# Kernel tuning notes

Measured on AMD Instinct MI355X. Metric: run time of the kernel, lower is better.

## Reference

```python
import jax, jax.numpy as jnp
import numpy as np

N = 100000   # nodes
E = 800000   # edges
F_IN = 16
H = 64       # hidden_dim
L = 4        # num_layers
CD = 8       # contrastive_dim
BN_EPS = 1e-5


def setup_inputs() -> dict:
    key = jax.random.key(0)
    ks = jax.random.split(key, 20)
    s = 0.05
    return {
        "x": jax.random.normal(ks[0], (N, F_IN), jnp.float32),
        "edge_index": jax.random.randint(ks[1], (2, E), 0, N, jnp.int64),
        "batch": jnp.zeros((N,), jnp.int64),
        "enc_w1": jax.random.normal(ks[2], (F_IN, H), jnp.float32) * s,
        "enc_b1": jnp.zeros((H,), jnp.float32),
        "enc_w2": jax.random.normal(ks[3], (H, H), jnp.float32) * s,
        "enc_b2": jnp.zeros((H,), jnp.float32),
        "conv_w": jax.random.normal(ks[4], (L, 2 * H, H), jnp.float32) * s,
        "conv_b": jnp.zeros((L, H), jnp.float32),
        "bn_gamma": jnp.ones((L, H), jnp.float32),
        "bn_beta": jnp.zeros((L, H), jnp.float32),
        "out_w1": jax.random.normal(ks[5], (H, 64), jnp.float32) * s,
        "out_b1": jnp.zeros((64,), jnp.float32),
        "out_w2": jax.random.normal(ks[6], (64, 32), jnp.float32) * s,
        "out_b2": jnp.zeros((32,), jnp.float32),
        "out_w3": jax.random.normal(ks[7], (32, CD), jnp.float32) * s,
        "out_b3": jnp.zeros((CD,), jnp.float32),
    }


def _forward(x, edge_index, enc_w1, enc_b1, enc_w2, enc_b2,
             conv_w, conv_b, bn_gamma, bn_beta,
             out_w1, out_b1, out_w2, out_b2, out_w3, out_b3):
    row, col = edge_index[0], edge_index[1]
    # lc_encode: Linear+ELU, Linear+ELU
    h = jax.nn.elu(x @ enc_w1 + enc_b1)
    feats = jax.nn.elu(h @ enc_w2 + enc_b2)  # (N, H)

    ones = jnp.ones((E, 1), feats.dtype)
    counts = jnp.clip(jax.ops.segment_sum(ones, row, num_segments=N), 1.0)  # (N,1)
    bn_scale = 1.0 / jnp.sqrt(1.0 + BN_EPS)  # eval-mode BN: running_mean=0, running_var=1

    for i in range(L):
        xc = feats[row]               # gather centers (E, H)
        xn = feats[col]               # gather neighbors (E, H)
        ef = jnp.concatenate([xc, xn - xc], axis=-1)      # (E, 2H)
        e = jax.nn.elu(ef @ conv_w[i] + conv_b[i])        # Linear + ELU
        e = (e * bn_scale) * bn_gamma[i] + bn_beta[i]     # BatchNorm (eval); Dropout is identity
        agg = jax.ops.segment_sum(e, row, num_segments=N) / counts
        feats = agg + feats  # residual in Net.forward

    # output head (Dropout identity in eval)
    o = jax.nn.elu(feats @ out_w1 + out_b1)
    o = jax.nn.elu(o @ out_w2 + out_b2)
    return o @ out_w3 + out_b3  # (N, CD)


def reference(x, edge_index, batch, enc_w1, enc_b1, enc_w2, enc_b2,
              conv_w, conv_b, bn_gamma, bn_beta,
              out_w1, out_b1, out_w2, out_b2, out_w3, out_b3):
    out = _forward(x, edge_index, enc_w1, enc_b1, enc_w2, enc_b2,
                   conv_w, conv_b, bn_gamma, bn_beta,
                   out_w1, out_b1, out_w2, out_b2, out_w3, out_b3)
    return (out, batch)
```

## Files before the change

kernel.cpp:

```cpp
#include <hip/hip_runtime.h>

#define NN 100000
#define NE 800000
#define FIN 16
#define H 64
#define NL 4
#define CDIM 8
#define NT 1563
#define ROWS_PER_OWN 12500
#define ECHUNK 2048
#define NCHUNK ((NE + ECHUNK - 1) / ECHUNK)
#define CAP 32
#define HOT 8
#define SPILL (CAP - HOT)

__device__ __forceinline__ float elu(float x) { return x > 0.f ? x : __expf(x) - 1.f; }
__device__ __forceinline__ float4 elu4(float4 v) {
    return make_float4(elu(v.x), elu(v.y), elu(v.z), elu(v.w));
}

__device__ __forceinline__ unsigned short f2bf(float x) {
    union { float f; unsigned int u; } v; v.f = x;
    unsigned int r = v.u + 0x7fffu + ((v.u >> 16) & 1u);
    return (unsigned short)(r >> 16);
}
__device__ __forceinline__ float u2f(unsigned int u) {
    union { unsigned int u; float f; } v; v.u = u;
    return v.f;
}

__global__ __launch_bounds__(256) void k_scatter(const int* __restrict__ row,
                                                 const int* __restrict__ col,
                                                 int* cnt, int* __restrict__ hot,
                                                 int* __restrict__ spill) {
    int owner = blockIdx.x & 7;
    int chunk = blockIdx.x >> 3;
    int lo = owner * ROWS_PER_OWN, hi = lo + ROWS_PER_OWN;
    int base = chunk * ECHUNK;
    int end = base + ECHUNK; if (end > NE) end = NE;
    for (int e = base + threadIdx.x; e < end; e += 256) {
        int r = row[e];
        if (r >= lo && r < hi) {
            int p = atomicAdd(&cnt[r], 1);
            if (p < HOT) hot[(size_t)r * HOT + p] = col[e];
            else if (p < CAP) spill[(size_t)r * SPILL + (p - HOT)] = col[e];
        }
    }
}

__global__ __launch_bounds__(256) void k_enc(const float* __restrict__ x,
                                             const float* __restrict__ w1,
                                             const float* __restrict__ b1,
                                             const float* __restrict__ w2,
                                             const float* __restrict__ b2,
                                             float* __restrict__ feats,
                                             int* __restrict__ cnt) {
    __shared__ __align__(16) float xs[64 * 16];
    __shared__ __align__(16) float w1s[16 * 64];
    __shared__ __align__(16) float ws[64 * 64];
    __shared__ __align__(16) float fs[64 * 68];
    int tid = threadIdx.x;
    int base = blockIdx.x * 64;
    {
        int gid = blockIdx.x * 256 + tid;
        if (gid < NN) cnt[gid] = 0;
    }
    {
        size_t ei = (size_t)base * FIN + tid * 4;
        size_t emax = (size_t)NN * FIN - 4;
        if (ei > emax) ei = emax;
        *(float4*)&xs[tid * 4] = *(const float4*)&x[ei];
    }
    ((float4*)w1s)[tid] = ((const float4*)w1)[tid];
#pragma unroll
    for (int r = 0; r < 4; r++) ((float4*)ws)[tid + 256 * r] = ((const float4*)w2)[tid + 256 * r];
    __syncthreads();

    int wave = tid >> 6, j = tid & 63;
    float bb1 = b1[j];
    for (int i = 0; i < 16; i++) {
        int nl = i * 4 + wave;
        float acc = bb1;
#pragma unroll
        for (int k = 0; k < FIN; k++) acc += xs[nl * FIN + k] * w1s[k * 64 + j];
        fs[nl * 68 + j] = elu(acc);
    }
    __syncthreads();

    int cg = tid & 15, ng = tid >> 4;
    int c0 = cg * 4;
    float4 bb = ((const float4*)b2)[cg];
    float4 acc[4];
    acc[0] = bb; acc[1] = bb; acc[2] = bb; acc[3] = bb;
#pragma unroll 2
    for (int kq = 0; kq < 16; kq++) {
        int k0 = kq * 4;
        float4 w0 = *(const float4*)&ws[(k0 + 0) * 64 + c0];
        float4 w1v = *(const float4*)&ws[(k0 + 1) * 64 + c0];
        float4 w2v = *(const float4*)&ws[(k0 + 2) * 64 + c0];
        float4 w3v = *(const float4*)&ws[(k0 + 3) * 64 + c0];
#pragma unroll
        for (int m = 0; m < 4; m++) {
            float4 f = *(const float4*)&fs[(ng * 4 + m) * 68 + k0];
            acc[m].x += f.x * w0.x + f.y * w1v.x + f.z * w2v.x + f.w * w3v.x;
            acc[m].y += f.x * w0.y + f.y * w1v.y + f.z * w2v.y + f.w * w3v.y;
            acc[m].z += f.x * w0.z + f.y * w1v.z + f.z * w2v.z + f.w * w3v.z;
            acc[m].w += f.x * w0.w + f.y * w1v.w + f.z * w2v.w + f.w * w3v.w;
        }
    }
#pragma unroll
    for (int m = 0; m < 4; m++) {
        int n = base + ng * 4 + m;
        if (n < NN) *(float4*)&feats[(size_t)n * 64 + c0] = elu4(acc[m]);
    }
}

__global__ __launch_bounds__(256) void k_ab(const float* __restrict__ feats,
                                            const float* __restrict__ convw,
                                            const float* __restrict__ convb,
                                            unsigned short* __restrict__ Am,
                                            unsigned short* __restrict__ Bm) {
    __shared__ __align__(16) float fs[64 * 68];
    __shared__ __align__(16) float was[64 * 64];
    __shared__ __align__(16) float wbs[64 * 64];
    int tid = threadIdx.x;
    int base = blockIdx.x * 64;
#pragma unroll
    for (int r = 0; r < 4; r++) {
        int idx = tid + 256 * r;
        float4 wt = ((const float4*)convw)[idx];
        float4 wb = ((const float4*)convw)[1024 + idx];
        ((float4*)was)[idx] = make_float4(wt.x - wb.x, wt.y - wb.y, wt.z - wb.z, wt.w - wb.w);
        ((float4*)wbs)[idx] = wb;
        int rw = idx >> 4, cc = idx & 15;
        int n = base + rw; if (n >= NN) n = NN - 1;
        *(float4*)&fs[rw * 68 + cc * 4] = *(const float4*)&feats[(size_t)n * 64 + cc * 4];
    }
    __syncthreads();
    int cg = tid & 15, ng = tid >> 4;
    int c0 = cg * 4;
    float4 cb = ((const float4*)convb)[cg];
    float4 z = make_float4(0.f, 0.f, 0.f, 0.f);
    float4 accA[4], accB[4];
    accA[0] = cb; accA[1] = cb; accA[2] = cb; accA[3] = cb;
    accB[0] = z; accB[1] = z; accB[2] = z; accB[3] = z;
#pragma unroll 1
    for (int kq = 0; kq < 16; kq++) {
        int k0 = kq * 4;
        float4 a0 = *(const float4*)&was[(k0 + 0) * 64 + c0];
        float4 a1 = *(const float4*)&was[(k0 + 1) * 64 + c0];
        float4 a2 = *(const float4*)&was[(k0 + 2) * 64 + c0];
        float4 a3 = *(const float4*)&was[(k0 + 3) * 64 + c0];
        float4 b0 = *(const float4*)&wbs[(k0 + 0) * 64 + c0];
        float4 b1v = *(const float4*)&wbs[(k0 + 1) * 64 + c0];
        float4 b2v = *(const float4*)&wbs[(k0 + 2) * 64 + c0];
        float4 b3v = *(const float4*)&wbs[(k0 + 3) * 64 + c0];
#pragma unroll
        for (int m = 0; m < 4; m++) {
            float4 f = *(const float4*)&fs[(ng * 4 + m) * 68 + k0];
            accA[m].x += f.x * a0.x + f.y * a1.x + f.z * a2.x + f.w * a3.x;
            accA[m].y += f.x * a0.y + f.y * a1.y + f.z * a2.y + f.w * a3.y;
            accA[m].z += f.x * a0.z + f.y * a1.z + f.z * a2.z + f.w * a3.z;
            accA[m].w += f.x * a0.w + f.y * a1.w + f.z * a2.w + f.w * a3.w;
            accB[m].x += f.x * b0.x + f.y * b1v.x + f.z * b2v.x + f.w * b3v.x;
            accB[m].y += f.x * b0.y + f.y * b1v.y + f.z * b2v.y + f.w * b3v.y;
            accB[m].z += f.x * b0.z + f.y * b1v.z + f.z * b2v.z + f.w * b3v.z;
            accB[m].w += f.x * b0.w + f.y * b1v.w + f.z * b2v.w + f.w * b3v.w;
        }
    }
#pragma unroll
    for (int m = 0; m < 4; m++) {
        int n = base + ng * 4 + m;
        if (n < NN) {
            ushort4 pa, pb;
            pa.x = f2bf(accA[m].x); pa.y = f2bf(accA[m].y);
            pa.z = f2bf(accA[m].z); pa.w = f2bf(accA[m].w);
            pb.x = f2bf(accB[m].x); pb.y = f2bf(accB[m].y);
            pb.z = f2bf(accB[m].z); pb.w = f2bf(accB[m].w);
            *(ushort4*)&Am[(size_t)n * 64 + c0] = pa;
            *(ushort4*)&Bm[(size_t)n * 64 + c0] = pb;
        }
    }
}

__global__ __launch_bounds__(256) void k_gather(const unsigned short* __restrict__ Am,
                                                const unsigned short* __restrict__ Bm,
                                                const int* __restrict__ cnt,
                                                const int* __restrict__ hot,
                                                const int* __restrict__ spill,
                                                const float* __restrict__ gamma,
                                                const float* __restrict__ beta,
                                                float* __restrict__ feats) {
    int tid = threadIdx.x;
    int wave = tid >> 6, lane = tid & 63;
    int half = lane >> 5, l = lane & 31;
    int n = blockIdx.x * 8 + wave * 2 + half;
    int g = l >> 3;
    int cq = l & 7, c0 = cq * 8;
    int deg = cnt[n];
    if (deg > CAP) deg = CAP;
    int mycol = (l < HOT) ? hot[(size_t)n * HOT + l]
                          : spill[(size_t)n * SPILL + (l - HOT)];
    uint4 rawA = *(const uint4*)&Am[(size_t)n * H + c0];
    float4 a0 = make_float4(u2f(rawA.x << 16), u2f(rawA.x & 0xffff0000u),
                            u2f(rawA.y << 16), u2f(rawA.y & 0xffff0000u));
    float4 a1 = make_float4(u2f(rawA.z << 16), u2f(rawA.z & 0xffff0000u),
                            u2f(rawA.w << 16), u2f(rawA.w & 0xffff0000u));
    float4 f0, f1;
    if (g == 0) {
        f0 = *(const float4*)&feats[(size_t)n * H + c0];
        f1 = *(const float4*)&feats[(size_t)n * H + c0 + 4];
    }
    float4 acc0 = make_float4(0.f, 0.f, 0.f, 0.f);
    float4 acc1 = make_float4(0.f, 0.f, 0.f, 0.f);
    for (int p0 = 0; p0 < deg; p0 += 4) {
        int p = p0 + g;
        bool valid = p < deg;
        int pc = valid ? p : (deg - 1);
        int c = __shfl(mycol, (half << 5) + pc);
        uint4 raw = *(const uint4*)&Bm[(size_t)c * H + c0];
        float4 b0 = make_float4(u2f(raw.x << 16), u2f(raw.x & 0xffff0000u),
                                u2f(raw.y << 16), u2f(raw.y & 0xffff0000u));
        float4 b1 = make_float4(u2f(raw.z << 16), u2f(raw.z & 0xffff0000u),
                                u2f(raw.w << 16), u2f(raw.w & 0xffff0000u));
        float4 v0 = elu4(make_float4(a0.x + b0.x, a0.y + b0.y, a0.z + b0.z, a0.w + b0.w));
        float4 v1 = elu4(make_float4(a1.x + b1.x, a1.y + b1.y, a1.z + b1.z, a1.w + b1.w));
        if (valid) {
            acc0.x += v0.x; acc0.y += v0.y; acc0.z += v0.z; acc0.w += v0.w;
            acc1.x += v1.x; acc1.y += v1.y; acc1.z += v1.z; acc1.w += v1.w;
        }
    }
#pragma unroll
    for (int d = 8; d < 32; d <<= 1) {
        acc0.x += __shfl_xor(acc0.x, d); acc0.y += __shfl_xor(acc0.y, d);
        acc0.z += __shfl_xor(acc0.z, d); acc0.w += __shfl_xor(acc0.w, d);
        acc1.x += __shfl_xor(acc1.x, d); acc1.y += __shfl_xor(acc1.y, d);
        acc1.z += __shfl_xor(acc1.z, d); acc1.w += __shfl_xor(acc1.w, d);
    }
    if (g == 0 && deg > 0) {
        const float bs = 0.99999500003749968750f;
        float inv = bs / (float)deg;
        float4 gm0 = *(const float4*)&gamma[c0];
        float4 gm1 = *(const float4*)&gamma[c0 + 4];
        float4 bt0 = *(const float4*)&beta[c0];
        float4 bt1 = *(const float4*)&beta[c0 + 4];
        f0.x += acc0.x * gm0.x * inv + bt0.x;
        f0.y += acc0.y * gm0.y * inv + bt0.y;
        f0.z += acc0.z * gm0.z * inv + bt0.z;
        f0.w += acc0.w * gm0.w * inv + bt0.w;
        f1.x += acc1.x * gm1.x * inv + bt1.x;
        f1.y += acc1.y * gm1.y * inv + bt1.y;
        f1.z += acc1.z * gm1.z * inv + bt1.z;
        f1.w += acc1.w * gm1.w * inv + bt1.w;
        *(float4*)&feats[(size_t)n * H + c0] = f0;
        *(float4*)&feats[(size_t)n * H + c0 + 4] = f1;
    }
}

__global__ __launch_bounds__(256) void k_head(const float* __restrict__ feats,
                                              const float* __restrict__ w1,
                                              const float* __restrict__ b1,
                                              const float* __restrict__ w2,
                                              const float* __restrict__ b2,
                                              const float* __restrict__ w3,
                                              const float* __restrict__ b3,
                                              const int* __restrict__ batch,
                                              float* __restrict__ out,
                                              float* __restrict__ out2) {
    __shared__ __align__(16) float fs[64 * 68];
    __shared__ __align__(16) float w1s[64 * 64];
    __shared__ __align__(16) float o1s[64 * 68];
    __shared__ __align__(16) float w2s[64 * 32];
    __shared__ __align__(16) float w3s[32 * 8];
    int tid = threadIdx.x;
    int base = blockIdx.x * 64;
#pragma unroll
    for (int r = 0; r < 4; r++) {
        int idx = tid + 256 * r;
        ((float4*)w1s)[idx] = ((const float4*)w1)[idx];
        int rw = idx >> 4, cc = idx & 15;
        int n = base + rw; if (n >= NN) n = NN - 1;
        *(float4*)&fs[rw * 68 + cc * 4] = *(const float4*)&feats[(size_t)n * 64 + cc * 4];
    }
    ((float4*)w2s)[tid] = ((const float4*)w2)[tid];
    ((float4*)w2s)[tid + 256] = ((const float4*)w2)[tid + 256];
    if (tid < 64) ((float4*)w3s)[tid] = ((const float4*)w3)[tid];
    if (tid < 64) {
        int n = base + tid;
        if (n < NN) out2[n] = (float)batch[n];
    }
    __syncthreads();

    int cg = tid & 15, ng = tid >> 4;
    int c0 = cg * 4;
    {
        float4 bb = ((const float4*)b1)[cg];
        float4 acc[4];
        acc[0] = bb; acc[1] = bb; acc[2] = bb; acc[3] = bb;
#pragma unroll 2
        for (int kq = 0; kq < 16; kq++) {
            int k0 = kq * 4;
            float4 w0 = *(const float4*)&w1s[(k0 + 0) * 64 + c0];
            float4 w1v = *(const float4*)&w1s[(k0 + 1) * 64 + c0];
            float4 w2v = *(const float4*)&w1s[(k0 + 2) * 64 + c0];
            float4 w3v = *(const float4*)&w1s[(k0 + 3) * 64 + c0];
#pragma unroll
            for (int m = 0; m < 4; m++) {
                float4 f = *(const float4*)&fs[(ng * 4 + m) * 68 + k0];
                acc[m].x += f.x * w0.x + f.y * w1v.x + f.z * w2v.x + f.w * w3v.x;
                acc[m].y += f.x * w0.y + f.y * w1v.y + f.z * w2v.y + f.w * w3v.y;
                acc[m].z += f.x * w0.z + f.y * w1v.z + f.z * w2v.z + f.w * w3v.z;
                acc[m].w += f.x * w0.w + f.y * w1v.w + f.z * w2v.w + f.w * w3v.w;
            }
        }
        __syncthreads();
#pragma unroll
        for (int m = 0; m < 4; m++)
            *(float4*)&o1s[(ng * 4 + m) * 68 + c0] = elu4(acc[m]);
    }
    __syncthreads();

    float* o2s = fs;
    {
        int cg2 = tid & 7, ng2 = tid >> 3;
        int c20 = cg2 * 4;
        float4 bb = ((const float4*)b2)[cg2];
        float4 acc[2];
        acc[0] = bb; acc[1] = bb;
#pragma unroll 2
        for (int kq = 0; kq < 16; kq++) {
            int k0 = kq * 4;
            float4 w0 = *(const float4*)&w2s[(k0 + 0) * 32 + c20];
            float4 w1v = *(const float4*)&w2s[(k0 + 1) * 32 + c20];
            float4 w2v = *(const float4*)&w2s[(k0 + 2) * 32 + c20];
            float4 w3v = *(const float4*)&w2s[(k0 + 3) * 32 + c20];
#pragma unroll
            for (int m = 0; m < 2; m++) {
                float4 f = *(const float4*)&o1s[(ng2 * 2 + m) * 68 + k0];
                acc[m].x += f.x * w0.x + f.y * w1v.x + f.z * w2v.x + f.w * w3v.x;
                acc[m].y += f.x * w0.y + f.y * w1v.y + f.z * w2v.y + f.w * w3v.y;
                acc[m].z += f.x * w0.z + f.y * w1v.z + f.z * w2v.z + f.w * w3v.z;
                acc[m].w += f.x * w0.w + f.y * w1v.w + f.z * w2v.w + f.w * w3v.w;
            }
        }
#pragma unroll
        for (int m = 0; m < 2; m++)
            *(float4*)&o2s[(ng2 * 2 + m) * 40 + c20] = elu4(acc[m]);
    }
    __syncthreads();

    if (tid < 128) {
        int n3 = tid >> 1, c30 = (tid & 1) * 4;
        float4 acc = ((const float4*)b3)[tid & 1];
#pragma unroll 2
        for (int kq = 0; kq < 8; kq++) {
            int k0 = kq * 4;
            float4 w0 = *(const float4*)&w3s[(k0 + 0) * 8 + c30];
            float4 w1v = *(const float4*)&w3s[(k0 + 1) * 8 + c30];
            float4 w2v = *(const float4*)&w3s[(k0 + 2) * 8 + c30];
            float4 w3v = *(const float4*)&w3s[(k0 + 3) * 8 + c30];
            float4 f = *(const float4*)&o2s[n3 * 40 + k0];
            acc.x += f.x * w0.x + f.y * w1v.x + f.z * w2v.x + f.w * w3v.x;
            acc.y += f.x * w0.y + f.y * w1v.y + f.z * w2v.y + f.w * w3v.y;
            acc.z += f.x * w0.z + f.y * w1v.z + f.z * w2v.z + f.w * w3v.z;
            acc.w += f.x * w0.w + f.y * w1v.w + f.z * w2v.w + f.w * w3v.w;
        }
        int n = base + n3;
        if (n < NN) *(float4*)&out[(size_t)n * 8 + c30] = acc;
    }
}

extern "C" void kernel_launch(void* const* d_in, const int* in_sizes, int n_in,
                              void* d_out, int out_size, void* d_ws, size_t ws_size,
                              hipStream_t stream) {
    const float* x = (const float*)d_in[0];
    const int* edge_index = (const int*)d_in[1];
    const int* batch = (const int*)d_in[2];
    const float* enc_w1 = (const float*)d_in[3];
    const float* enc_b1 = (const float*)d_in[4];
    const float* enc_w2 = (const float*)d_in[5];
    const float* enc_b2 = (const float*)d_in[6];
    const float* conv_w = (const float*)d_in[7];
    const float* conv_b = (const float*)d_in[8];
    const float* bn_gamma = (const float*)d_in[9];
    const float* bn_beta = (const float*)d_in[10];
    const float* out_w1 = (const float*)d_in[11];
    const float* out_b1 = (const float*)d_in[12];
    const float* out_w2 = (const float*)d_in[13];
    const float* out_b2 = (const float*)d_in[14];
    const float* out_w3 = (const float*)d_in[15];
    const float* out_b3 = (const float*)d_in[16];

    const int* row = edge_index;
    const int* col = edge_index + NE;

    float* feats = (float*)d_ws;
    unsigned short* Abuf = (unsigned short*)(feats + (size_t)NN * H);
    unsigned short* Bbuf = Abuf + (size_t)NN * H;
    int* cnt = (int*)(Bbuf + (size_t)NN * H);
    int* hot = cnt + NN;
    int* spill = hot + (size_t)NN * HOT;

    float* out = (float*)d_out;

    k_enc<<<NT, 256, 0, stream>>>(x, enc_w1, enc_b1, enc_w2, enc_b2, feats, cnt);
    k_scatter<<<NCHUNK * 8, 256, 0, stream>>>(row, col, cnt, hot, spill);

    for (int i = 0; i < NL; i++) {
        k_ab<<<NT, 256, 0, stream>>>(feats, conv_w + (size_t)i * 2 * H * H,
                                     conv_b + (size_t)i * H, Abuf, Bbuf);
        k_gather<<<NN / 8, 256, 0, stream>>>(Abuf, Bbuf, cnt, hot, spill,
                                             bn_gamma + (size_t)i * H,
                                             bn_beta + (size_t)i * H, feats);
    }

    k_head<<<NT, 256, 0, stream>>>(feats, out_w1, out_b1, out_w2, out_b2,
                                   out_w3, out_b3, batch, out,
                                   out + (size_t)NN * CDIM);
}
```

Before: 416.2 us.

## Compute per-node A/B projections with bf16 MFMA using pre-transposed weights

Weight differencing and transposition into a bf16 layout are precomputed once for all layers by extra blocks appended to the scatter kernel. The per-layer node projection kernel then runs 16x16x32 bf16 MFMA instructions with weights held in registers, instead of fp32 FMAs over shared memory tiles. It processes 128 nodes per block, has no shared-memory staging or block barrier, and converts feats to bf16 on the fly. This is meant to cut the ALU and LDS cost of the dense projection. It adds bf16 rounding of inputs and weights before accumulation.

```diff
diff --git a/kernel.cpp b/kernel.cpp
--- a/kernel.cpp
+++ b/kernel.cpp
@@ -7,6 +7,7 @@
 #define NL 4
 #define CDIM 8
 #define NT 1563
+#define NAB 782
 #define ROWS_PER_OWN 12500
 #define ECHUNK 2048
 #define NCHUNK ((NE + ECHUNK - 1) / ECHUNK)
@@ -14,6 +15,9 @@
 #define HOT 8
 #define SPILL (CAP - HOT)
 
+typedef __attribute__((ext_vector_type(8))) short bf16x8;
+typedef __attribute__((ext_vector_type(4))) float f32x4;
+
 __device__ __forceinline__ float elu(float x) { return x > 0.f ? x : __expf(x) - 1.f; }
 __device__ __forceinline__ float4 elu4(float4 v) {
     return make_float4(elu(v.x), elu(v.y), elu(v.z), elu(v.w));
@@ -32,7 +36,28 @@
 __global__ __launch_bounds__(256) void k_scatter(const int* __restrict__ row,
                                                  const int* __restrict__ col,
                                                  int* cnt, int* __restrict__ hot,
-                                                 int* __restrict__ spill) {
+                                                 int* __restrict__ spill,
+                                                 const float* __restrict__ convw,
+                                                 unsigned short* __restrict__ WT) {
+    if (blockIdx.x >= NCHUNK * 8) {
+        int t = (blockIdx.x - NCHUNK * 8) * 256 + threadIdx.x;
+        int i = t >> 11;
+        int rem = t & 2047;
+        int j = rem >> 4;
+        int kg = rem & 15;
+        const float* W = convw + (size_t)i * 2 * H * H;
+        float v[4];
+#pragma unroll
+        for (int q = 0; q < 4; q++) {
+            int k = kg * 4 + q;
+            if (j < 64) v[q] = W[k * 64 + j] - W[(64 + k) * 64 + j];
+            else        v[q] = W[(64 + k) * 64 + (j - 64)];
+        }
+        ushort4 p;
+        p.x = f2bf(v[0]); p.y = f2bf(v[1]); p.z = f2bf(v[2]); p.w = f2bf(v[3]);
+        *(ushort4*)&WT[(size_t)i * 8192 + j * 64 + kg * 4] = p;
+        return;
+    }
     int owner = blockIdx.x & 7;
     int chunk = blockIdx.x >> 3;
     int lo = owner * ROWS_PER_OWN, hi = lo + ROWS_PER_OWN;
@@ -116,69 +141,68 @@
 }
 
 __global__ __launch_bounds__(256) void k_ab(const float* __restrict__ feats,
-                                            const float* __restrict__ convw,
+                                            const unsigned short* __restrict__ WT,
                                             const float* __restrict__ convb,
                                             unsigned short* __restrict__ Am,
                                             unsigned short* __restrict__ Bm) {
-    __shared__ __align__(16) float fs[64 * 68];
-    __shared__ __align__(16) float was[64 * 64];
-    __shared__ __align__(16) float wbs[64 * 64];
     int tid = threadIdx.x;
-    int base = blockIdx.x * 64;
-#pragma unroll
-    for (int r = 0; r < 4; r++) {
-        int idx = tid + 256 * r;
-        float4 wt = ((const float4*)convw)[idx];
-        float4 wb = ((const float4*)convw)[1024 + idx];
-        ((float4*)was)[idx] = make_float4(wt.x - wb.x, wt.y - wb.y, wt.z - wb.z, wt.w - wb.w);
-        ((float4*)wbs)[idx] = wb;
-        int rw = idx >> 4, cc = idx & 15;
-        int n = base + rw; if (n >= NN) n = NN - 1;
-        *(float4*)&fs[rw * 68 + cc * 4] = *(const float4*)&feats[(size_t)n * 64 + cc * 4];
-    }
-    __syncthreads();
-    int cg = tid & 15, ng = tid >> 4;
-    int c0 = cg * 4;
-    float4 cb = ((const float4*)convb)[cg];
-    float4 z = make_float4(0.f, 0.f, 0.f, 0.f);
-    float4 accA[4], accB[4];
-    accA[0] = cb; accA[1] = cb; accA[2] = cb; accA[3] = cb;
-    accB[0] = z; accB[1] = z; accB[2] = z; accB[3] = z;
-#pragma unroll 1
-    for (int kq = 0; kq < 16; kq++) {
-        int k0 = kq * 4;
-        float4 a0 = *(const float4*)&was[(k0 + 0) * 64 + c0];
-        float4 a1 = *(const float4*)&was[(k0 + 1) * 64 + c0];
-        float4 a2 = *(const float4*)&was[(k0 + 2) * 64 + c0];
-        float4 a3 = *(const float4*)&was[(k0 + 3) * 64 + c0];
-        float4 b0 = *(const float4*)&wbs[(k0 + 0) * 64 + c0];
-        float4 b1v = *(const float4*)&wbs[(k0 + 1) * 64 + c0];
-        float4 b2v = *(const float4*)&wbs[(k0 + 2) * 64 + c0];
-        float4 b3v = *(const float4*)&wbs[(k0 + 3) * 64 + c0];
-#pragma unroll
-        for (int m = 0; m < 4; m++) {
-            float4 f = *(const float4*)&fs[(ng * 4 + m) * 68 + k0];
-            accA[m].x += f.x * a0.x + f.y * a1.x + f.z * a2.x + f.w * a3.x;
-            accA[m].y += f.x * a0.y + f.y * a1.y + f.z * a2.y + f.w * a3.y;
-            accA[m].z += f.x * a0.z + f.y * a1.z + f.z * a2.z + f.w * a3.z;
-            accA[m].w += f.x * a0.w + f.y * a1.w + f.z * a2.w + f.w * a3.w;
-            accB[m].x += f.x * b0.x + f.y * b1v.x + f.z * b2v.x + f.w * b3v.x;
-            accB[m].y += f.x * b0.y + f.y * b1v.y + f.z * b2v.y + f.w * b3v.y;
-            accB[m].z += f.x * b0.z + f.y * b1v.z + f.z * b2v.z + f.w * b3v.z;
-            accB[m].w += f.x * b0.w + f.y * b1v.w + f.z * b2v.w + f.w * b3v.w;
-        }
-    }
-#pragma unroll
-    for (int m = 0; m < 4; m++) {
-        int n = base + ng * 4 + m;
+    int wave = tid >> 6, l = tid & 63;
+    int lr = l & 15;
+    int lk = l >> 4;
+    int nb = blockIdx.x * 128 + wave * 32;
+
+    bf16x8 wf[8][2];
+#pragma unroll
+    for (int ct = 0; ct < 8; ct++)
+#pragma unroll
+        for (int kt = 0; kt < 2; kt++)
+            wf[ct][kt] = *(const bf16x8*)&WT[(ct * 16 + lr) * 64 + kt * 32 + lk * 8];
+
+    f32x4 acc[2][8];
+#pragma unroll
+    for (int ct = 0; ct < 4; ct++) {
+        float4 bq = *(const float4*)&convb[ct * 16 + lk * 4];
+        f32x4 bv; bv[0] = bq.x; bv[1] = bq.y; bv[2] = bq.z; bv[3] = bq.w;
+        f32x4 z = (f32x4)(0.0f);
+        acc[0][ct] = bv; acc[1][ct] = bv;
+        acc[0][ct + 4] = z; acc[1][ct + 4] = z;
+    }
+
+#pragma unroll
+    for (int nt = 0; nt < 2; nt++) {
+        int n = nb + nt * 16 + lr; if (n >= NN) n = NN - 1;
+        bf16x8 ff[2];
+#pragma unroll
+        for (int kt = 0; kt < 2; kt++) {
+            float4 f0 = *(const float4*)&feats[(size_t)n * 64 + kt * 32 + lk * 8];
+            float4 f1 = *(const float4*)&feats[(size_t)n * 64 + kt * 32 + lk * 8 + 4];
+            bf16x8 t;
+            t[0] = (short)f2bf(f0.x); t[1] = (short)f2bf(f0.y);
+            t[2] = (short)f2bf(f0.z); t[3] = (short)f2bf(f0.w);
+            t[4] = (short)f2bf(f1.x); t[5] = (short)f2bf(f1.y);
+            t[6] = (short)f2bf(f1.z); t[7] = (short)f2bf(f1.w);
+            ff[kt] = t;
+        }
+#pragma unroll
+        for (int ct = 0; ct < 8; ct++) {
+            acc[nt][ct] = __builtin_amdgcn_mfma_f32_16x16x32_bf16(wf[ct][0], ff[0], acc[nt][ct], 0, 0, 0);
+            acc[nt][ct] = __builtin_amdgcn_mfma_f32_16x16x32_bf16(wf[ct][1], ff[1], acc[nt][ct], 0, 0, 0);
+        }
+    }
+
+#pragma unroll
+    for (int nt = 0; nt < 2; nt++) {
+        int n = nb + nt * 16 + lr;
         if (n < NN) {
-            ushort4 pa, pb;
-            pa.x = f2bf(accA[m].x); pa.y = f2bf(accA[m].y);
-            pa.z = f2bf(accA[m].z); pa.w = f2bf(accA[m].w);
-            pb.x = f2bf(accB[m].x); pb.y = f2bf(accB[m].y);
-            pb.z = f2bf(accB[m].z); pb.w = f2bf(accB[m].w);
-            *(ushort4*)&Am[(size_t)n * 64 + c0] = pa;
-            *(ushort4*)&Bm[(size_t)n * 64 + c0] = pb;
+#pragma unroll
+            for (int ct = 0; ct < 8; ct++) {
+                ushort4 p;
+                p.x = f2bf(acc[nt][ct][0]); p.y = f2bf(acc[nt][ct][1]);
+                p.z = f2bf(acc[nt][ct][2]); p.w = f2bf(acc[nt][ct][3]);
+                unsigned short* dst = (ct < 4) ? Am : Bm;
+                int wc = (ct & 3) * 16 + lk * 4;
+                *(ushort4*)&dst[(size_t)n * 64 + wc] = p;
+            }
         }
     }
 }
@@ -400,15 +424,16 @@
     int* cnt = (int*)(Bbuf + (size_t)NN * H);
     int* hot = cnt + NN;
     int* spill = hot + (size_t)NN * HOT;
+    unsigned short* WT = (unsigned short*)(spill + (size_t)NN * SPILL);
 
     float* out = (float*)d_out;
 
     k_enc<<<NT, 256, 0, stream>>>(x, enc_w1, enc_b1, enc_w2, enc_b2, feats, cnt);
-    k_scatter<<<NCHUNK * 8, 256, 0, stream>>>(row, col, cnt, hot, spill);
+    k_scatter<<<NCHUNK * 8 + 32, 256, 0, stream>>>(row, col, cnt, hot, spill, conv_w, WT);
 
     for (int i = 0; i < NL; i++) {
-        k_ab<<<NT, 256, 0, stream>>>(feats, conv_w + (size_t)i * 2 * H * H,
-                                     conv_b + (size_t)i * H, Abuf, Bbuf);
+        k_ab<<<NAB, 256, 0, stream>>>(feats, WT + (size_t)i * 8192,
+                                      conv_b + (size_t)i * H, Abuf, Bbuf);
         k_gather<<<NN / 8, 256, 0, stream>>>(Abuf, Bbuf, cnt, hot, spill,
                                              bn_gamma + (size_t)i * H,
                                              bn_beta + (size_t)i * H, feats);
```

Measured after the change: 383.6 us. 1.09x faster.
